# Kernel optimization log

Measured on AMD Instinct MI355X. Metric: run time of the kernel, lower is better.

The kernel has to match this reference:

```python
import jax, jax.numpy as jnp
import numpy as np

KERNEL_SIZE = 3


def setup_inputs() -> dict:
    key = jax.random.key(0)
    k1, k2 = jax.random.split(key)
    x = jax.random.normal(k1, (4, 64, 256, 256), dtype=jnp.float32)
    kernel = jax.random.normal(k2, (4, KERNEL_SIZE * KERNEL_SIZE, 256, 256), dtype=jnp.float32)
    return {"x": x, "kernel": kernel}


def reference(x, kernel):
    # x: [b, c, h, w]; kernel: [b, k*k, h, w]
    b, c, h, w = x.shape
    k = KERNEL_SIZE
    p = k // 2
    # nn.ReflectionPad2d(k//2)
    xp = jnp.pad(x, ((0, 0), (0, 0), (p, p), (p, p)), mode="reflect")
    # softmax over the k*k dimension (dim=1)
    kw = jax.nn.softmax(kernel, axis=1)  # [b, k*k, h, w]
    # Fused gather-multiply-reduce: instead of materializing the k^2-expanded
    # unfold tensor, accumulate over the k*k shifted views. Unfold ordering is
    # row-major over (dy, dx), matching index i = dy*k + dx.
    out = jnp.zeros_like(x)
    for dy in range(k):
        for dx in range(k):
            patch = xp[:, :, dy:dy + h, dx:dx + w]          # [b, c, h, w]
            out = out + kw[:, dy * k + dx][:, None] * patch  # broadcast over c
    return out
```

## Files before the change

kernel.cpp:

```cpp
#include <hip/hip_runtime.h>
#include <stdint.h>


constexpr int BATCH = 4;
constexpr int CHAN  = 64;
constexpr int HH    = 256;
constexpr int WW    = 256;
constexpr int CG    = 4;
constexpr int RPB   = 4;
constexpr int NROW  = RPB + 2;

typedef float vf4 __attribute__((ext_vector_type(4)));

typedef const __attribute__((address_space(1))) void* gas_ptr;
typedef __attribute__((address_space(3))) void* las_ptr;

__global__ __launch_bounds__(256) void dynconv_kernel(
    const float* __restrict__ x,
    const float* __restrict__ ker,
    float* __restrict__ out)
{
    __shared__ float lds[CG][NROW][WW];

    const int t  = threadIdx.x;
    const int rb = t >> 6;
    const int wq = t & 63;
    const int w0 = wq * 4;

    const int hband = blockIdx.x;
    const int cg    = blockIdx.y;
    const int b     = blockIdx.z;
    const int h0    = hband * RPB;
    const int h     = h0 + rb;

    const long cs = (long)HH * WW;
    const float* xb = x   + (((long)b * CHAN + cg * CG) * cs);
    float*       ob = out + (((long)b * CHAN + cg * CG) * cs);

    #pragma unroll
    for (int k = 0; k < (CG * NROW) / RPB; ++k) {
        const int idx  = k * RPB + rb;
        const int ch   = idx / NROW;
        const int slot = idx % NROW;
        int g = h0 - 1 + slot;
        g = (g < 0) ? 1 : ((g > HH - 1) ? HH - 2 : g);
        const float* gsrc = xb + (long)ch * cs + (long)g * WW + w0;
        __builtin_amdgcn_global_load_lds((gas_ptr)gsrc, (las_ptr)&lds[ch][slot][0], 16, 0, 0);
    }

    float kv[9][4];
    const long kbase = (((long)b * 9) * HH + h) * WW + w0;
    #pragma unroll
    for (int j = 0; j < 9; ++j) {
        const float4 v = *reinterpret_cast<const float4*>(ker + kbase + (long)j * HH * WW);
        kv[j][0] = v.x; kv[j][1] = v.y; kv[j][2] = v.z; kv[j][3] = v.w;
    }
    #pragma unroll
    for (int p = 0; p < 4; ++p) {
        float m = kv[0][p];
        #pragma unroll
        for (int j = 1; j < 9; ++j) m = fmaxf(m, kv[j][p]);
        float s = 0.f;
        #pragma unroll
        for (int j = 0; j < 9; ++j) { kv[j][p] = __expf(kv[j][p] - m); s += kv[j][p]; }
        const float inv = 1.0f / s;
        #pragma unroll
        for (int j = 0; j < 9; ++j) kv[j][p] *= inv;
    }

    __syncthreads();

    #pragma unroll
    for (int i = 0; i < CG; ++i) {
        float acc0 = 0.f, acc1 = 0.f, acc2 = 0.f, acc3 = 0.f;
        #pragma unroll
        for (int r = 0; r < 3; ++r) {
            const float4 v = *reinterpret_cast<const float4*>(&lds[i][rb + r][w0]);
            float lft = __shfl_up(v.w, 1);
            if (wq == 0)  lft = v.y;
            float rgt = __shfl_down(v.x, 1);
            if (wq == 63) rgt = v.z;
            const float vals[6] = { lft, v.x, v.y, v.z, v.w, rgt };
            #pragma unroll
            for (int dx = 0; dx < 3; ++dx) {
                const int j = r * 3 + dx;
                acc0 = fmaf(kv[j][0], vals[0 + dx], acc0);
                acc1 = fmaf(kv[j][1], vals[1 + dx], acc1);
                acc2 = fmaf(kv[j][2], vals[2 + dx], acc2);
                acc3 = fmaf(kv[j][3], vals[3 + dx], acc3);
            }
        }
        vf4 o; o.x = acc0; o.y = acc1; o.z = acc2; o.w = acc3;
        __builtin_nontemporal_store(o, reinterpret_cast<vf4*>(ob + (long)i * cs + (long)h * WW + w0));
    }
}

extern "C" void kernel_launch(void* const* d_in, const int* in_sizes, int n_in,
                              void* d_out, int out_size, void* d_ws, size_t ws_size,
                              hipStream_t stream) {
    const float* x   = (const float*)d_in[0];
    const float* ker = (const float*)d_in[1];
    float* out = (float*)d_out;

    dim3 grid(HH / RPB, CHAN / CG, BATCH);
    dim3 block(256);
    dynconv_kernel<<<grid, block, 0, stream>>>(x, ker, out);
}
```

Baseline: 31.36 us.

## Precompute softmax weights in a separate kernel and read halo from LDS

Adds a pre-pass kernel that computes the 9-way softmax once per pixel and writes normalized weights to workspace. The conv kernel then loads the ready weights, so the softmax is no longer recomputed by each of the 16 channel-group blocks. Halo neighbours are now read straight from LDS instead of through wave shuffles. The cost is an extra launch plus a workspace write and read of the weights. If the workspace is too small, the code falls back to the fused kernel.

```diff
diff --git a/kernel.cpp b/kernel.cpp
--- a/kernel.cpp
+++ b/kernel.cpp
@@ -9,15 +9,49 @@
 constexpr int CG    = 4;
 constexpr int RPB   = 4;
 constexpr int NROW  = RPB + 2;
+constexpr long WS_ELEMS = (long)BATCH * 9 * HH * WW;
 
 typedef float vf4 __attribute__((ext_vector_type(4)));
-
 typedef const __attribute__((address_space(1))) void* gas_ptr;
 typedef __attribute__((address_space(3))) void* las_ptr;
 
-__global__ __launch_bounds__(256) void dynconv_kernel(
+__global__ __launch_bounds__(256) void softmax_kernel(
+    const float* __restrict__ ker, float* __restrict__ wsw)
+{
+    const int tid = blockIdx.x * 256 + threadIdx.x;
+    const int wq  = tid & 63;
+    const int hh  = (tid >> 6) & (HH - 1);
+    const int bb  = tid >> 14;
+    const long base = (((long)bb * 9) * HH + hh) * WW + wq * 4;
+
+    float kv[9][4];
+    #pragma unroll
+    for (int j = 0; j < 9; ++j) {
+        const float4 v = *reinterpret_cast<const float4*>(ker + base + (long)j * HH * WW);
+        kv[j][0] = v.x; kv[j][1] = v.y; kv[j][2] = v.z; kv[j][3] = v.w;
+    }
+    #pragma unroll
+    for (int p = 0; p < 4; ++p) {
+        float m = kv[0][p];
+        #pragma unroll
+        for (int j = 1; j < 9; ++j) m = fmaxf(m, kv[j][p]);
+        float s = 0.f;
+        #pragma unroll
+        for (int j = 0; j < 9; ++j) { kv[j][p] = __expf(kv[j][p] - m); s += kv[j][p]; }
+        const float inv = 1.0f / s;
+        #pragma unroll
+        for (int j = 0; j < 9; ++j) kv[j][p] *= inv;
+    }
+    #pragma unroll
+    for (int j = 0; j < 9; ++j) {
+        vf4 o; o.x = kv[j][0]; o.y = kv[j][1]; o.z = kv[j][2]; o.w = kv[j][3];
+        *reinterpret_cast<vf4*>(wsw + base + (long)j * HH * WW) = o;
+    }
+}
+
+__global__ __launch_bounds__(256) void conv_kernel(
     const float* __restrict__ x,
-    const float* __restrict__ ker,
+    const float* __restrict__ wsr,
     float* __restrict__ out)
 {
     __shared__ float lds[CG][NROW][WW];
@@ -52,20 +86,8 @@
     const long kbase = (((long)b * 9) * HH + h) * WW + w0;
     #pragma unroll
     for (int j = 0; j < 9; ++j) {
-        const float4 v = *reinterpret_cast<const float4*>(ker + kbase + (long)j * HH * WW);
+        const float4 v = *reinterpret_cast<const float4*>(wsr + kbase + (long)j * HH * WW);
         kv[j][0] = v.x; kv[j][1] = v.y; kv[j][2] = v.z; kv[j][3] = v.w;
-    }
-    #pragma unroll
-    for (int p = 0; p < 4; ++p) {
-        float m = kv[0][p];
-        #pragma unroll
-        for (int j = 1; j < 9; ++j) m = fmaxf(m, kv[j][p]);
-        float s = 0.f;
-        #pragma unroll
-        for (int j = 0; j < 9; ++j) { kv[j][p] = __expf(kv[j][p] - m); s += kv[j][p]; }
-        const float inv = 1.0f / s;
-        #pragma unroll
-        for (int j = 0; j < 9; ++j) kv[j][p] *= inv;
     }
 
     __syncthreads();
@@ -75,11 +97,10 @@
         float acc0 = 0.f, acc1 = 0.f, acc2 = 0.f, acc3 = 0.f;
         #pragma unroll
         for (int r = 0; r < 3; ++r) {
-            const float4 v = *reinterpret_cast<const float4*>(&lds[i][rb + r][w0]);
-            float lft = __shfl_up(v.w, 1);
-            if (wq == 0)  lft = v.y;
-            float rgt = __shfl_down(v.x, 1);
-            if (wq == 63) rgt = v.z;
+            const float* lrow = &lds[i][rb + r][0];
+            const float4 v = *reinterpret_cast<const float4*>(lrow + w0);
+            const float lft = lrow[(wq == 0)  ? 1      : w0 - 1];
+            const float rgt = lrow[(wq == 63) ? WW - 2 : w0 + 4];
             const float vals[6] = { lft, v.x, v.y, v.z, v.w, rgt };
             #pragma unroll
             for (int dx = 0; dx < 3; ++dx) {
@@ -95,6 +116,85 @@
     }
 }
 
+__global__ __launch_bounds__(256) void dynconv_fused_kernel(
+    const float* __restrict__ x,
+    const float* __restrict__ ker,
+    float* __restrict__ out)
+{
+    __shared__ float lds[CG][NROW][WW];
+
+    const int t  = threadIdx.x;
+    const int rb = t >> 6;
+    const int wq = t & 63;
+    const int w0 = wq * 4;
+
+    const int hband = blockIdx.x;
+    const int cg    = blockIdx.y;
+    const int b     = blockIdx.z;
+    const int h0    = hband * RPB;
+    const int h     = h0 + rb;
+
+    const long cs = (long)HH * WW;
+    const float* xb = x   + (((long)b * CHAN + cg * CG) * cs);
+    float*       ob = out + (((long)b * CHAN + cg * CG) * cs);
+
+    #pragma unroll
+    for (int k = 0; k < (CG * NROW) / RPB; ++k) {
+        const int idx  = k * RPB + rb;
+        const int ch   = idx / NROW;
+        const int slot = idx % NROW;
+        int g = h0 - 1 + slot;
+        g = (g < 0) ? 1 : ((g > HH - 1) ? HH - 2 : g);
+        const float* gsrc = xb + (long)ch * cs + (long)g * WW + w0;
+        __builtin_amdgcn_global_load_lds((gas_ptr)gsrc, (las_ptr)&lds[ch][slot][0], 16, 0, 0);
+    }
+
+    float kv[9][4];
+    const long kbase = (((long)b * 9) * HH + h) * WW + w0;
+    #pragma unroll
+    for (int j = 0; j < 9; ++j) {
+        const float4 v = *reinterpret_cast<const float4*>(ker + kbase + (long)j * HH * WW);
+        kv[j][0] = v.x; kv[j][1] = v.y; kv[j][2] = v.z; kv[j][3] = v.w;
+    }
+    #pragma unroll
+    for (int p = 0; p < 4; ++p) {
+        float m = kv[0][p];
+        #pragma unroll
+        for (int j = 1; j < 9; ++j) m = fmaxf(m, kv[j][p]);
+        float s = 0.f;
+        #pragma unroll
+        for (int j = 0; j < 9; ++j) { kv[j][p] = __expf(kv[j][p] - m); s += kv[j][p]; }
+        const float inv = 1.0f / s;
+        #pragma unroll
+        for (int j = 0; j < 9; ++j) kv[j][p] *= inv;
+    }
+
+    __syncthreads();
+
+    #pragma unroll
+    for (int i = 0; i < CG; ++i) {
+        float acc0 = 0.f, acc1 = 0.f, acc2 = 0.f, acc3 = 0.f;
+        #pragma unroll
+        for (int r = 0; r < 3; ++r) {
+            const float* lrow = &lds[i][rb + r][0];
+            const float4 v = *reinterpret_cast<const float4*>(lrow + w0);
+            const float lft = lrow[(wq == 0)  ? 1      : w0 - 1];
+            const float rgt = lrow[(wq == 63) ? WW - 2 : w0 + 4];
+            const float vals[6] = { lft, v.x, v.y, v.z, v.w, rgt };
+            #pragma unroll
+            for (int dx = 0; dx < 3; ++dx) {
+                const int j = r * 3 + dx;
+                acc0 = fmaf(kv[j][0], vals[0 + dx], acc0);
+                acc1 = fmaf(kv[j][1], vals[1 + dx], acc1);
+                acc2 = fmaf(kv[j][2], vals[2 + dx], acc2);
+                acc3 = fmaf(kv[j][3], vals[3 + dx], acc3);
+            }
+        }
+        vf4 o; o.x = acc0; o.y = acc1; o.z = acc2; o.w = acc3;
+        __builtin_nontemporal_store(o, reinterpret_cast<vf4*>(ob + (long)i * cs + (long)h * WW + w0));
+    }
+}
+
 extern "C" void kernel_launch(void* const* d_in, const int* in_sizes, int n_in,
                               void* d_out, int out_size, void* d_ws, size_t ws_size,
                               hipStream_t stream) {
@@ -102,7 +202,13 @@
     const float* ker = (const float*)d_in[1];
     float* out = (float*)d_out;
 
-    dim3 grid(HH / RPB, CHAN / CG, BATCH);
-    dim3 block(256);
-    dynconv_kernel<<<grid, block, 0, stream>>>(x, ker, out);
-}
+    if (ws_size >= WS_ELEMS * sizeof(float)) {
+        float* wsw = (float*)d_ws;
+        softmax_kernel<<<dim3(256), dim3(256), 0, stream>>>(ker, wsw);
+        dim3 grid(HH / RPB, CHAN / CG, BATCH);
+        conv_kernel<<<grid, dim3(256), 0, stream>>>(x, wsw, out);
+    } else {
+        dim3 grid(HH / RPB, CHAN / CG, BATCH);
+        dynconv_fused_kernel<<<grid, dim3(256), 0, stream>>>(x, ker, out);
+    }
+}
```

New measurement: 39.08 us. 1.25x slower.
